# Kernel optimization log

Measured on AMD Instinct MI355X. Metric: run time of the kernel, lower is better.

## Reference

```python
import jax, jax.numpy as jnp
import numpy as np

N, K = 200000, 16
C_IN = 4           # in_channels (head stage)
H1, H2 = 16, 32    # nbr_hidden_channels//2, nbr_hidden_channels
C_OUT = 64         # channel_list[0]
HEAD = 256         # head_channels
EPS = 1e-5


def _bn(x, g, b):
    # train-mode BatchNorm1d over the row (point/neighbor) axis
    m = jnp.mean(x, axis=0)
    v = jnp.var(x, axis=0)
    return (x - m) * jax.lax.rsqrt(v + EPS) * g + b


def setup_inputs() -> dict:
    key = jax.random.key(0)
    ks = jax.random.split(key, 8)

    def lin(k, fan_in, fan_out):
        bound = 1.0 / np.sqrt(fan_in)  # torch Linear default init
        return jax.random.uniform(k, (fan_in, fan_out), minval=-bound, maxval=bound, dtype=jnp.float32)

    return {
        "p": jax.random.normal(ks[0], (N, 3), dtype=jnp.float32),
        "f": jax.random.normal(ks[1], (N, C_IN), dtype=jnp.float32),
        "group_idx": jax.random.randint(ks[2], (N, K), 0, N),
        "w1": lin(ks[3], 3 + C_IN, H1),
        "g1": jnp.ones((H1,), jnp.float32),
        "b1": jnp.zeros((H1,), jnp.float32),
        "w2": lin(ks[4], H1, H2),
        "g2": jnp.ones((H2,), jnp.float32),
        "b2": jnp.zeros((H2,), jnp.float32),
        "w3": lin(ks[5], H2, C_OUT),
        "g_nbr": 0.8 * jnp.ones((C_OUT,), jnp.float32),  # nn.init.constant_(nbr_bn.weight, 0.8)
        "b_nbr": jnp.zeros((C_OUT,), jnp.float32),
        "g_post": jnp.ones((C_OUT,), jnp.float32),       # (channel_list[0]/out_channels)**0.5 == 1.0
        "b_post": jnp.zeros((C_OUT,), jnp.float32),
        "w_post": lin(ks[6], C_OUT, HEAD),
    }


def reference(p, f, group_idx, w1, g1, b1, w2, g2, b2, w3, g_nbr, b_nbr, g_post, b_post, w_post):
    # neighbor gather: relative coords and features  -> (N, K, 3), (N, K, C_IN)
    p_nbr = p[group_idx] - p[:, None, :]
    f_nbr = f[group_idx]
    x = jnp.concatenate([p_nbr, f_nbr], axis=-1).reshape(N * K, 3 + C_IN)
    # nbr_embed: Linear-BN-GELU x2 + Linear (all no-bias linears)
    x = jax.nn.gelu(_bn(x @ w1, g1, b1), approximate=False)
    x = jax.nn.gelu(_bn(x @ w2, g2, b2), approximate=False)
    x = (x @ w3).reshape(N, K, C_OUT).max(axis=1)  # max-pool over K neighbors
    # nbr_proj is Identity for the head stage; nbr_bn then f = f_nbr
    x = _bn(x, g_nbr, b_nbr)
    # post_proj: BN + Linear(C_OUT -> HEAD, no bias)
    out = _bn(x, g_post, b_post) @ w_post
    return out
```

## Files before the change

kernel.cpp:

```cpp
#include <hip/hip_runtime.h>
#include <cmath>

#define NPTS  200000
#define KNBR  16
#define MROWS 3200000
#define EPSB  1e-5f
#define H2LD  260

__device__ __forceinline__ float gelu_f(float x) {
    return 0.5f * x * (1.0f + erff(x * 0.70710678118654752f));
}

__global__ __launch_bounds__(256) void k_pack(
    const float* __restrict__ p, const float4* __restrict__ f,
    float4* __restrict__ pk)
{
    int n = blockIdx.x * 256 + threadIdx.x;
    if (n < NPTS) {
        float4 a;
        a.x = p[n * 3 + 0]; a.y = p[n * 3 + 1]; a.z = p[n * 3 + 2]; a.w = 0.f;
        pk[2 * n]     = a;
        pk[2 * n + 1] = f[n];
    }
}

__global__ __launch_bounds__(256) void k_gy1(
    const float4* __restrict__ pk, const int* __restrict__ gidx,
    const float* __restrict__ w1, float* __restrict__ stats,
    float* __restrict__ y1d)
{
    __shared__ __align__(16) float w1s[112];
    __shared__ float red[4 * 32];
    for (int i = threadIdx.x; i < 112; i += 256) w1s[i] = w1[i];
    __syncthreads();
    const float4* w1v = (const float4*)w1s;

    float acc[32];
#pragma unroll
    for (int c = 0; c < 32; c++) acc[c] = 0.f;

    int tid = threadIdx.x;
    int lr = tid & 63;
    int stride = gridDim.x * 256;
    for (int r = blockIdx.x * 256 + tid; r < MROWS; r += stride) {
        int n = r >> 4;
        int idx = gidx[r];
        float4 pa = pk[2 * idx];
        float4 fb = pk[2 * idx + 1];
        float4 pc = pk[2 * n];
        float x[7];
        x[0] = pa.x - pc.x; x[1] = pa.y - pc.y; x[2] = pa.z - pc.z;
        x[3] = fb.x; x[4] = fb.y; x[5] = fb.z; x[6] = fb.w;
        float* yb = y1d + (size_t)(r >> 6) * 1024 + lr;
#pragma unroll
        for (int j0 = 0; j0 < 16; j0 += 4) {
            float y0 = 0.f, y1 = 0.f, y2 = 0.f, y3 = 0.f;
#pragma unroll
            for (int i = 0; i < 7; i++) {
                float4 w = w1v[i * 4 + (j0 >> 2)];
                float xi = x[i];
                y0 = fmaf(xi, w.x, y0); y1 = fmaf(xi, w.y, y1);
                y2 = fmaf(xi, w.z, y2); y3 = fmaf(xi, w.w, y3);
            }
            yb[(j0 + 0) * 64] = y0; yb[(j0 + 1) * 64] = y1;
            yb[(j0 + 2) * 64] = y2; yb[(j0 + 3) * 64] = y3;
            acc[j0 + 0] += y0; acc[16 + j0 + 0] += y0 * y0;
            acc[j0 + 1] += y1; acc[16 + j0 + 1] += y1 * y1;
            acc[j0 + 2] += y2; acc[16 + j0 + 2] += y2 * y2;
            acc[j0 + 3] += y3; acc[16 + j0 + 3] += y3 * y3;
        }
    }
    int lane = tid & 63, wv = tid >> 6;
#pragma unroll
    for (int c = 0; c < 32; c++) {
        float v = acc[c];
        v += __shfl_down(v, 32); v += __shfl_down(v, 16); v += __shfl_down(v, 8);
        v += __shfl_down(v, 4);  v += __shfl_down(v, 2);  v += __shfl_down(v, 1);
        if (lane == 0) red[wv * 32 + c] = v;
    }
    __syncthreads();
    for (int c = tid; c < 32; c += 256)
        atomicAdd(&stats[c], red[c] + red[32 + c] + red[64 + c] + red[96 + c]);
}

__global__ void k_fin1b(const float* __restrict__ stats, const float* __restrict__ g,
                        const float* __restrict__ b, float* __restrict__ scsh)
{
    int j = threadIdx.x;
    if (j < 16) {
        const float invM = 1.0f / (float)MROWS;
        float m = stats[j] * invM;
        float v = stats[16 + j] * invM - m * m;
        float sc = g[j] * rsqrtf(v + EPSB);
        scsh[j] = sc;
        scsh[16 + j] = fmaf(-m, sc, b[j]);
    }
}

__global__ __launch_bounds__(256) void k_momA(
    const float* __restrict__ y1d, const float* __restrict__ scsh1,
    float* __restrict__ stats)
{
    __shared__ float sc1s[16], sh1s[16];
    __shared__ float red[4 * 81];
    if (threadIdx.x < 16) {
        sc1s[threadIdx.x] = scsh1[threadIdx.x];
        sh1s[threadIdx.x] = scsh1[16 + threadIdx.x];
    }
    __syncthreads();

    float acc[81];
#pragma unroll
    for (int c = 0; c < 81; c++) acc[c] = 0.f;

    int tid = threadIdx.x;
    int lr = tid & 63;
    int stride = gridDim.x * 256;
    for (int r = blockIdx.x * 256 + tid; r < MROWS; r += stride) {
        const float* yb = y1d + (size_t)(r >> 6) * 1024 + lr;
        float h1[16];
#pragma unroll
        for (int j = 0; j < 16; j++)
            h1[j] = gelu_f(fmaf(yb[j * 64], sc1s[j], sh1s[j]));
        int t = 0;
#pragma unroll
        for (int i = 0; i < 6; i++)
#pragma unroll
            for (int l = i; l < 16; l++) { acc[t] = fmaf(h1[i], h1[l], acc[t]); t++; }
    }
    int lane = tid & 63, wv = tid >> 6;
#pragma unroll
    for (int c = 0; c < 81; c++) {
        float v = acc[c];
        v += __shfl_down(v, 32); v += __shfl_down(v, 16); v += __shfl_down(v, 8);
        v += __shfl_down(v, 4);  v += __shfl_down(v, 2);  v += __shfl_down(v, 1);
        if (lane == 0) red[wv * 81 + c] = v;
    }
    __syncthreads();
    for (int c = tid; c < 81; c += 256)
        atomicAdd(&stats[c], red[c] + red[81 + c] + red[162 + c] + red[243 + c]);
}

__global__ __launch_bounds__(256) void k_momB(
    const float* __restrict__ y1d, const float* __restrict__ scsh1,
    float* __restrict__ stats)
{
    __shared__ float sc1s[16], sh1s[16];
    __shared__ float red[4 * 71];
    if (threadIdx.x < 16) {
        sc1s[threadIdx.x] = scsh1[threadIdx.x];
        sh1s[threadIdx.x] = scsh1[16 + threadIdx.x];
    }
    __syncthreads();

    float acc[71];
#pragma unroll
    for (int c = 0; c < 71; c++) acc[c] = 0.f;

    int tid = threadIdx.x;
    int lr = tid & 63;
    int stride = gridDim.x * 256;
    for (int r = blockIdx.x * 256 + tid; r < MROWS; r += stride) {
        const float* yb = y1d + (size_t)(r >> 6) * 1024 + lr;
        float h1[16];
#pragma unroll
        for (int j = 0; j < 16; j++)
            h1[j] = gelu_f(fmaf(yb[j * 64], sc1s[j], sh1s[j]));
#pragma unroll
        for (int i = 0; i < 16; i++) acc[i] += h1[i];
        int t = 16;
#pragma unroll
        for (int i = 6; i < 16; i++)
#pragma unroll
            for (int l = i; l < 16; l++) { acc[t] = fmaf(h1[i], h1[l], acc[t]); t++; }
    }
    int lane = tid & 63, wv = tid >> 6;
#pragma unroll
    for (int c = 0; c < 71; c++) {
        float v = acc[c];
        v += __shfl_down(v, 32); v += __shfl_down(v, 16); v += __shfl_down(v, 8);
        v += __shfl_down(v, 4);  v += __shfl_down(v, 2);  v += __shfl_down(v, 1);
        if (lane == 0) red[wv * 71 + c] = v;
    }
    __syncthreads();
    for (int c = tid; c < 71; c += 256)
        atomicAdd(&stats[81 + c], red[c] + red[71 + c] + red[142 + c] + red[213 + c]);
}

__global__ void k_fin2(const float* __restrict__ stats, const float* __restrict__ w2,
                       const float* __restrict__ g, const float* __restrict__ b,
                       float* __restrict__ scsh)
{
    int j = threadIdx.x;
    if (j < 32) {
        const float invM = 1.0f / (float)MROWS;
        float w[16];
#pragma unroll
        for (int i = 0; i < 16; i++) w[i] = w2[i * 32 + j];
        float m = 0.f;
#pragma unroll
        for (int i = 0; i < 16; i++) m = fmaf(w[i], stats[81 + i], m);
        m *= invM;
        float e2 = 0.f;
        int t = 0;
#pragma unroll
        for (int i = 0; i < 6; i++)
#pragma unroll
            for (int l = i; l < 16; l++) {
                float coeff = (i == l) ? 1.0f : 2.0f;
                e2 = fmaf(coeff * w[i] * w[l], stats[t], e2);
                t++;
            }
        t = 97;
#pragma unroll
        for (int i = 6; i < 16; i++)
#pragma unroll
            for (int l = i; l < 16; l++) {
                float coeff = (i == l) ? 1.0f : 2.0f;
                e2 = fmaf(coeff * w[i] * w[l], stats[t], e2);
                t++;
            }
        e2 *= invM;
        float v = e2 - m * m;
        float sc = g[j] * rsqrtf(v + EPSB);
        scsh[j] = sc;
        scsh[32 + j] = fmaf(-m, sc, b[j]);
    }
}

__global__ __launch_bounds__(256) void k_pool2y(
    const float* __restrict__ y1d,
    const float* __restrict__ w2, const float* __restrict__ w3,
    const float* __restrict__ scsh1, const float* __restrict__ scsh2,
    float* __restrict__ stats, float* __restrict__ pooled)
{
    __shared__ __align__(16) float w2s[512];
    __shared__ __align__(16) float w3s[2048];
    __shared__ __align__(16) float h2t[32 * H2LD];
    __shared__ float sc1s[16], sh1s[16], sc2s[32], sh2s[32];
    __shared__ float reds[256];
    __shared__ float redq[256];
    int tid = threadIdx.x;
    for (int i = tid; i < 512; i += 256) w2s[i] = w2[i];
    for (int i = tid; i < 2048; i += 256) w3s[i] = w3[i];
    if (tid < 16) { sc1s[tid] = scsh1[tid]; sh1s[tid] = scsh1[16 + tid]; }
    if (tid < 32) { sc2s[tid] = scsh2[tid]; sh2s[tid] = scsh2[32 + tid]; }
    __syncthreads();

    const float4* w2v = (const float4*)w2s;
    const float4* w3v = (const float4*)w3s;

    int lane = tid & 63;
    int pt = tid >> 4;
    int cc = tid & 15;

    float s0 = 0.f, s1 = 0.f, s2 = 0.f, s3 = 0.f;
    float q0 = 0.f, q1 = 0.f, q2 = 0.f, q3 = 0.f;

#pragma unroll 1
    for (int it = 0; it < 4; it++) {
        int r = it * 800000 + blockIdx.x * 256 + tid;
        const float* yb = y1d + (size_t)(r >> 6) * 1024 + lane;
        float h1[16];
#pragma unroll
        for (int j = 0; j < 16; j++)
            h1[j] = gelu_f(fmaf(yb[j * 64], sc1s[j], sh1s[j]));
#pragma unroll
        for (int j0 = 0; j0 < 32; j0 += 4) {
            float y0 = 0.f, y1 = 0.f, y2 = 0.f, y3 = 0.f;
#pragma unroll
            for (int i = 0; i < 16; i++) {
                float4 w = w2v[i * 8 + (j0 >> 2)];
                float hi = h1[i];
                y0 = fmaf(hi, w.x, y0); y1 = fmaf(hi, w.y, y1);
                y2 = fmaf(hi, w.z, y2); y3 = fmaf(hi, w.w, y3);
            }
            h2t[(j0 + 0) * H2LD + tid] = gelu_f(fmaf(y0, sc2s[j0 + 0], sh2s[j0 + 0]));
            h2t[(j0 + 1) * H2LD + tid] = gelu_f(fmaf(y1, sc2s[j0 + 1], sh2s[j0 + 1]));
            h2t[(j0 + 2) * H2LD + tid] = gelu_f(fmaf(y2, sc2s[j0 + 2], sh2s[j0 + 2]));
            h2t[(j0 + 3) * H2LD + tid] = gelu_f(fmaf(y3, sc2s[j0 + 3], sh2s[j0 + 3]));
        }
        __syncthreads();

        float a[16][4];
#pragma unroll
        for (int t = 0; t < 16; t++) {
            a[t][0] = 0.f; a[t][1] = 0.f; a[t][2] = 0.f; a[t][3] = 0.f;
        }
        int rb0 = pt << 4;
#pragma unroll 8
        for (int i = 0; i < 32; i++) {
            float4 wf = w3v[i * 16 + cc];
            const float* hrow = &h2t[i * H2LD + rb0];
            float4 hA = *(const float4*)&hrow[0];
            float4 hB = *(const float4*)&hrow[4];
            float4 hC = *(const float4*)&hrow[8];
            float4 hD = *(const float4*)&hrow[12];
            float hn[16] = { hA.x, hA.y, hA.z, hA.w,
                             hB.x, hB.y, hB.z, hB.w,
                             hC.x, hC.y, hC.z, hC.w,
                             hD.x, hD.y, hD.z, hD.w };
#pragma unroll
            for (int t = 0; t < 16; t++) {
                float h = hn[t];
                a[t][0] = fmaf(h, wf.x, a[t][0]);
                a[t][1] = fmaf(h, wf.y, a[t][1]);
                a[t][2] = fmaf(h, wf.z, a[t][2]);
                a[t][3] = fmaf(h, wf.w, a[t][3]);
            }
        }
        float m0 = -3.0e38f, m1 = -3.0e38f, m2 = -3.0e38f, m3 = -3.0e38f;
#pragma unroll
        for (int t = 0; t < 16; t++) {
            m0 = fmaxf(m0, a[t][0]);
            m1 = fmaxf(m1, a[t][1]);
            m2 = fmaxf(m2, a[t][2]);
            m3 = fmaxf(m3, a[t][3]);
        }
        int np = it * 50000 + blockIdx.x * 16 + pt;
        *(float4*)&pooled[(size_t)np * 64 + cc * 4] = make_float4(m0, m1, m2, m3);
        s0 += m0; q0 = fmaf(m0, m0, q0);
        s1 += m1; q1 = fmaf(m1, m1, q1);
        s2 += m2; q2 = fmaf(m2, m2, q2);
        s3 += m3; q3 = fmaf(m3, m3, q3);
        __syncthreads();
    }

    s0 += __shfl_down(s0, 32); s0 += __shfl_down(s0, 16);
    s1 += __shfl_down(s1, 32); s1 += __shfl_down(s1, 16);
    s2 += __shfl_down(s2, 32); s2 += __shfl_down(s2, 16);
    s3 += __shfl_down(s3, 32); s3 += __shfl_down(s3, 16);
    q0 += __shfl_down(q0, 32); q0 += __shfl_down(q0, 16);
    q1 += __shfl_down(q1, 32); q1 += __shfl_down(q1, 16);
    q2 += __shfl_down(q2, 32); q2 += __shfl_down(q2, 16);
    q3 += __shfl_down(q3, 32); q3 += __shfl_down(q3, 16);
    int wv = tid >> 6;
    if (lane < 16) {
        reds[wv * 64 + lane * 4 + 0] = s0;
        reds[wv * 64 + lane * 4 + 1] = s1;
        reds[wv * 64 + lane * 4 + 2] = s2;
        reds[wv * 64 + lane * 4 + 3] = s3;
        redq[wv * 64 + lane * 4 + 0] = q0;
        redq[wv * 64 + lane * 4 + 1] = q1;
        redq[wv * 64 + lane * 4 + 2] = q2;
        redq[wv * 64 + lane * 4 + 3] = q3;
    }
    __syncthreads();
    if (tid < 64) {
        atomicAdd(&stats[tid],
                  reds[tid] + reds[64 + tid] + reds[128 + tid] + reds[192 + tid]);
        atomicAdd(&stats[64 + tid],
                  redq[tid] + redq[64 + tid] + redq[128 + tid] + redq[192 + tid]);
    }
}

__global__ __launch_bounds__(256) void k_s1g(
    const float4* __restrict__ pk, const int* __restrict__ gidx,
    float* __restrict__ stats)
{
    __shared__ float red[4 * 35];
    float acc[35];
#pragma unroll
    for (int c = 0; c < 35; c++) acc[c] = 0.f;
    int stride = gridDim.x * 256;
    for (int r = blockIdx.x * 256 + threadIdx.x; r < MROWS; r += stride) {
        int n = r >> 4;
        int idx = gidx[r];
        float4 pa = pk[2 * idx];
        float4 fb = pk[2 * idx + 1];
        float4 pc = pk[2 * n];
        float x[7];
        x[0] = pa.x - pc.x; x[1] = pa.y - pc.y; x[2] = pa.z - pc.z;
        x[3] = fb.x; x[4] = fb.y; x[5] = fb.z; x[6] = fb.w;
#pragma unroll
        for (int i = 0; i < 7; i++) acc[i] += x[i];
        int t = 7;
#pragma unroll
        for (int i = 0; i < 7; i++)
#pragma unroll
            for (int l = i; l < 7; l++) { acc[t] = fmaf(x[i], x[l], acc[t]); t++; }
    }
    int lane = threadIdx.x & 63, wv = threadIdx.x >> 6;
#pragma unroll
    for (int c = 0; c < 35; c++) {
        float v = acc[c];
        v += __shfl_down(v, 32); v += __shfl_down(v, 16); v += __shfl_down(v, 8);
        v += __shfl_down(v, 4);  v += __shfl_down(v, 2);  v += __shfl_down(v, 1);
        if (lane == 0) red[wv * 35 + c] = v;
    }
    __syncthreads();
    for (int c = threadIdx.x; c < 35; c += 256)
        atomicAdd(&stats[c], red[c] + red[35 + c] + red[70 + c] + red[105 + c]);
}

__global__ void k_f1g(const float* __restrict__ stats, const float* __restrict__ w1,
                      const float* __restrict__ g, const float* __restrict__ b,
                      float* __restrict__ scsh)
{
    int j = threadIdx.x;
    if (j < 16) {
        const float invM = 1.0f / (float)MROWS;
        float w[7];
#pragma unroll
        for (int i = 0; i < 7; i++) w[i] = w1[i * 16 + j];
        float m = 0.f;
#pragma unroll
        for (int i = 0; i < 7; i++) m = fmaf(w[i], stats[i], m);
        m *= invM;
        float e2 = 0.f;
        int t = 7;
#pragma unroll
        for (int i = 0; i < 7; i++)
#pragma unroll
            for (int l = i; l < 7; l++) {
                float coeff = (i == l) ? 1.0f : 2.0f;
                e2 = fmaf(coeff * w[i] * w[l], stats[t], e2);
                t++;
            }
        e2 *= invM;
        float v = e2 - m * m;
        float sc = g[j] * rsqrtf(v + EPSB);
        scsh[j] = sc;
        scsh[16 + j] = fmaf(-m, sc, b[j]);
    }
}

template <int PASS>
__global__ __launch_bounds__(256) void k_s2g(
    const float4* __restrict__ pk, const int* __restrict__ gidx,
    const float* __restrict__ w1, const float* __restrict__ scsh1,
    float* __restrict__ stats)
{
    constexpr int NA = (PASS == 0) ? 81 : 71;
    __shared__ __align__(16) float w1s[112];
    __shared__ float sc1s[16], sh1s[16];
    __shared__ float red[4 * NA];
    for (int i = threadIdx.x; i < 112; i += 256) w1s[i] = w1[i];
    if (threadIdx.x < 16) {
        sc1s[threadIdx.x] = scsh1[threadIdx.x];
        sh1s[threadIdx.x] = scsh1[16 + threadIdx.x];
    }
    __syncthreads();
    const float4* w1v = (const float4*)w1s;

    float acc[NA];
#pragma unroll
    for (int c = 0; c < NA; c++) acc[c] = 0.f;

    int stride = gridDim.x * 256;
    for (int r = blockIdx.x * 256 + threadIdx.x; r < MROWS; r += stride) {
        int n = r >> 4;
        int idx = gidx[r];
        float4 pa = pk[2 * idx];
        float4 fb = pk[2 * idx + 1];
        float4 pc = pk[2 * n];
        float x[7];
        x[0] = pa.x - pc.x; x[1] = pa.y - pc.y; x[2] = pa.z - pc.z;
        x[3] = fb.x; x[4] = fb.y; x[5] = fb.z; x[6] = fb.w;
        float h1[16];
#pragma unroll
        for (int j0 = 0; j0 < 16; j0 += 4) {
            float y0 = 0.f, y1 = 0.f, y2 = 0.f, y3 = 0.f;
#pragma unroll
            for (int i = 0; i < 7; i++) {
                float4 w = w1v[i * 4 + (j0 >> 2)];
                float xi = x[i];
                y0 = fmaf(xi, w.x, y0); y1 = fmaf(xi, w.y, y1);
                y2 = fmaf(xi, w.z, y2); y3 = fmaf(xi, w.w, y3);
            }
            h1[j0 + 0] = gelu_f(fmaf(y0, sc1s[j0 + 0], sh1s[j0 + 0]));
            h1[j0 + 1] = gelu_f(fmaf(y1, sc1s[j0 + 1], sh1s[j0 + 1]));
            h1[j0 + 2] = gelu_f(fmaf(y2, sc1s[j0 + 2], sh1s[j0 + 2]));
            h1[j0 + 3] = gelu_f(fmaf(y3, sc1s[j0 + 3], sh1s[j0 + 3]));
        }
        if (PASS == 0) {
            int t = 0;
#pragma unroll
            for (int i = 0; i < 6; i++)
#pragma unroll
                for (int l = i; l < 16; l++) { acc[t] = fmaf(h1[i], h1[l], acc[t]); t++; }
        } else {
#pragma unroll
            for (int i = 0; i < 16; i++) acc[i] += h1[i];
            int t = 16;
#pragma unroll
            for (int i = 6; i < 16; i++)
#pragma unroll
                for (int l = i; l < 16; l++) { acc[t] = fmaf(h1[i], h1[l], acc[t]); t++; }
        }
    }
    int lane = threadIdx.x & 63, wv = threadIdx.x >> 6;
#pragma unroll
    for (int c = 0; c < NA; c++) {
        float v = acc[c];
        v += __shfl_down(v, 32); v += __shfl_down(v, 16); v += __shfl_down(v, 8);
        v += __shfl_down(v, 4);  v += __shfl_down(v, 2);  v += __shfl_down(v, 1);
        if (lane == 0) red[wv * NA + c] = v;
    }
    __syncthreads();
    int base = (PASS == 0) ? 0 : 81;
    for (int c = threadIdx.x; c < NA; c += 256)
        atomicAdd(&stats[base + c], red[c] + red[NA + c] + red[2 * NA + c] + red[3 * NA + c]);
}

__global__ __launch_bounds__(256) void k_pool2g(
    const float* __restrict__ p, const float4* __restrict__ f,
    const int* __restrict__ gidx,
    const float* __restrict__ w1, const float* __restrict__ w2,
    const float* __restrict__ w3,
    const float* __restrict__ scsh1, const float* __restrict__ scsh2,
    float* __restrict__ stats, float* __restrict__ pooled)
{
    __shared__ __align__(16) float w1s[112];
    __shared__ __align__(16) float w2s[512];
    __shared__ __align__(16) float w3s[2048];
    __shared__ __align__(16) float h2t[32 * H2LD];
    __shared__ float sc1s[16], sh1s[16], sc2s[32], sh2s[32];
    __shared__ float reds[256];
    __shared__ float redq[256];
    int tid = threadIdx.x;
    for (int i = tid; i < 112; i += 256) w1s[i] = w1[i];
    for (int i = tid; i < 512; i += 256) w2s[i] = w2[i];
    for (int i = tid; i < 2048; i += 256) w3s[i] = w3[i];
    if (tid < 16) { sc1s[tid] = scsh1[tid]; sh1s[tid] = scsh1[16 + tid]; }
    if (tid < 32) { sc2s[tid] = scsh2[tid]; sh2s[tid] = scsh2[32 + tid]; }
    __syncthreads();

    const float4* w1v = (const float4*)w1s;
    const float4* w2v = (const float4*)w2s;
    const float4* w3v = (const float4*)w3s;

    int lane = tid & 63;
    int pt = tid >> 4;
    int cc = tid & 15;

    float s0 = 0.f, s1 = 0.f, s2 = 0.f, s3 = 0.f;
    float q0 = 0.f, q1 = 0.f, q2 = 0.f, q3 = 0.f;

#pragma unroll 1
    for (int it = 0; it < 4; it++) {
        int r = it * 800000 + blockIdx.x * 256 + tid;
        int n = r >> 4;
        int idx = gidx[r];
        float4 fv = f[idx];
        float x[7];
        x[0] = p[idx * 3 + 0] - p[n * 3 + 0];
        x[1] = p[idx * 3 + 1] - p[n * 3 + 1];
        x[2] = p[idx * 3 + 2] - p[n * 3 + 2];
        x[3] = fv.x; x[4] = fv.y; x[5] = fv.z; x[6] = fv.w;

        float h1[16];
#pragma unroll
        for (int j0 = 0; j0 < 16; j0 += 4) {
            float y0 = 0.f, y1 = 0.f, y2 = 0.f, y3 = 0.f;
#pragma unroll
            for (int i = 0; i < 7; i++) {
                float4 w = w1v[i * 4 + (j0 >> 2)];
                float xi = x[i];
                y0 = fmaf(xi, w.x, y0); y1 = fmaf(xi, w.y, y1);
                y2 = fmaf(xi, w.z, y2); y3 = fmaf(xi, w.w, y3);
            }
            h1[j0 + 0] = gelu_f(fmaf(y0, sc1s[j0 + 0], sh1s[j0 + 0]));
            h1[j0 + 1] = gelu_f(fmaf(y1, sc1s[j0 + 1], sh1s[j0 + 1]));
            h1[j0 + 2] = gelu_f(fmaf(y2, sc1s[j0 + 2], sh1s[j0 + 2]));
            h1[j0 + 3] = gelu_f(fmaf(y3, sc1s[j0 + 3], sh1s[j0 + 3]));
        }
#pragma unroll
        for (int j0 = 0; j0 < 32; j0 += 4) {
            float y0 = 0.f, y1 = 0.f, y2 = 0.f, y3 = 0.f;
#pragma unroll
            for (int i = 0; i < 16; i++) {
                float4 w = w2v[i * 8 + (j0 >> 2)];
                float hi = h1[i];
                y0 = fmaf(hi, w.x, y0); y1 = fmaf(hi, w.y, y1);
                y2 = fmaf(hi, w.z, y2); y3 = fmaf(hi, w.w, y3);
            }
            h2t[(j0 + 0) * H2LD + tid] = gelu_f(fmaf(y0, sc2s[j0 + 0], sh2s[j0 + 0]));
            h2t[(j0 + 1) * H2LD + tid] = gelu_f(fmaf(y1, sc2s[j0 + 1], sh2s[j0 + 1]));
            h2t[(j0 + 2) * H2LD + tid] = gelu_f(fmaf(y2, sc2s[j0 + 2], sh2s[j0 + 2]));
            h2t[(j0 + 3) * H2LD + tid] = gelu_f(fmaf(y3, sc2s[j0 + 3], sh2s[j0 + 3]));
        }
        __syncthreads();

        float a[16][4];
#pragma unroll
        for (int t = 0; t < 16; t++) {
            a[t][0] = 0.f; a[t][1] = 0.f; a[t][2] = 0.f; a[t][3] = 0.f;
        }
        int rb0 = pt << 4;
#pragma unroll 8
        for (int i = 0; i < 32; i++) {
            float4 wf = w3v[i * 16 + cc];
            const float* hrow = &h2t[i * H2LD + rb0];
            float4 hA = *(const float4*)&hrow[0];
            float4 hB = *(const float4*)&hrow[4];
            float4 hC = *(const float4*)&hrow[8];
            float4 hD = *(const float4*)&hrow[12];
            float hn[16] = { hA.x, hA.y, hA.z, hA.w,
                             hB.x, hB.y, hB.z, hB.w,
                             hC.x, hC.y, hC.z, hC.w,
                             hD.x, hD.y, hD.z, hD.w };
#pragma unroll
            for (int t = 0; t < 16; t++) {
                float h = hn[t];
                a[t][0] = fmaf(h, wf.x, a[t][0]);
                a[t][1] = fmaf(h, wf.y, a[t][1]);
                a[t][2] = fmaf(h, wf.z, a[t][2]);
                a[t][3] = fmaf(h, wf.w, a[t][3]);
            }
        }
        float m0 = -3.0e38f, m1 = -3.0e38f, m2 = -3.0e38f, m3 = -3.0e38f;
#pragma unroll
        for (int t = 0; t < 16; t++) {
            m0 = fmaxf(m0, a[t][0]);
            m1 = fmaxf(m1, a[t][1]);
            m2 = fmaxf(m2, a[t][2]);
            m3 = fmaxf(m3, a[t][3]);
        }
        int np = it * 50000 + blockIdx.x * 16 + pt;
        *(float4*)&pooled[(size_t)np * 64 + cc * 4] = make_float4(m0, m1, m2, m3);
        s0 += m0; q0 = fmaf(m0, m0, q0);
        s1 += m1; q1 = fmaf(m1, m1, q1);
        s2 += m2; q2 = fmaf(m2, m2, q2);
        s3 += m3; q3 = fmaf(m3, m3, q3);
        __syncthreads();
    }

    s0 += __shfl_down(s0, 32); s0 += __shfl_down(s0, 16);
    s1 += __shfl_down(s1, 32); s1 += __shfl_down(s1, 16);
    s2 += __shfl_down(s2, 32); s2 += __shfl_down(s2, 16);
    s3 += __shfl_down(s3, 32); s3 += __shfl_down(s3, 16);
    q0 += __shfl_down(q0, 32); q0 += __shfl_down(q0, 16);
    q1 += __shfl_down(q1, 32); q1 += __shfl_down(q1, 16);
    q2 += __shfl_down(q2, 32); q2 += __shfl_down(q2, 16);
    q3 += __shfl_down(q3, 32); q3 += __shfl_down(q3, 16);
    int wv = tid >> 6;
    if (lane < 16) {
        reds[wv * 64 + lane * 4 + 0] = s0;
        reds[wv * 64 + lane * 4 + 1] = s1;
        reds[wv * 64 + lane * 4 + 2] = s2;
        reds[wv * 64 + lane * 4 + 3] = s3;
        redq[wv * 64 + lane * 4 + 0] = q0;
        redq[wv * 64 + lane * 4 + 1] = q1;
        redq[wv * 64 + lane * 4 + 2] = q2;
        redq[wv * 64 + lane * 4 + 3] = q3;
    }
    __syncthreads();
    if (tid < 64) {
        atomicAdd(&stats[tid],
                  reds[tid] + reds[64 + tid] + reds[128 + tid] + reds[192 + tid]);
        atomicAdd(&stats[64 + tid],
                  redq[tid] + redq[64 + tid] + redq[128 + tid] + redq[192 + tid]);
    }
}

__global__ void k_fin3(const float* __restrict__ stats,
                       const float* __restrict__ g_nbr, const float* __restrict__ g_post,
                       const float* __restrict__ b_post, float* __restrict__ scsh)
{
    int j = threadIdx.x;
    if (j < 64) {
        float m = stats[j] * (1.0f / NPTS);
        float v = stats[64 + j] * (1.0f / NPTS) - m * m;
        float a1 = g_nbr[j] * rsqrtf(v + EPSB);
        float s3 = g_post[j] * a1 * rsqrtf(fmaf(a1 * a1, v, EPSB));
        scsh[j] = s3;
        scsh[64 + j] = fmaf(-m, s3, b_post[j]);
    }
}

__global__ __launch_bounds__(256) void k_head(
    const float* __restrict__ pooled, const float* __restrict__ scsh3,
    const float* __restrict__ wpost, float* __restrict__ out)
{
    __shared__ float rowbuf[512];
    __shared__ float s3s[64], c3s[64];
    int tid = threadIdx.x;
    if (tid < 64) { s3s[tid] = scsh3[tid]; c3s[tid] = scsh3[64 + tid]; }
    float wcol[64];
#pragma unroll
    for (int j = 0; j < 64; j++) wcol[j] = wpost[j * 256 + tid];
    __syncthreads();

    const int nchunks = NPTS / 8;
    for (int c = blockIdx.x; c < nchunks; c += gridDim.x) {
        int n0 = c * 8;
#pragma unroll
        for (int t = tid; t < 512; t += 256) {
            int rr = t >> 6, j = t & 63;
            rowbuf[t] = fmaf(pooled[(size_t)(n0 + rr) * 64 + j], s3s[j], c3s[j]);
        }
        __syncthreads();
#pragma unroll
        for (int rr = 0; rr < 8; rr++) {
            float acc = 0.f;
#pragma unroll
            for (int j = 0; j < 64; j++) acc = fmaf(rowbuf[rr * 64 + j], wcol[j], acc);
            out[(size_t)(n0 + rr) * 256 + tid] = acc;
        }
        __syncthreads();
    }
}

extern "C" void kernel_launch(void* const* d_in, const int* in_sizes, int n_in,
                              void* d_out, int out_size, void* d_ws, size_t ws_size,
                              hipStream_t stream)
{
    const float*  p    = (const float*)d_in[0];
    const float4* f    = (const float4*)d_in[1];
    const int*    gidx = (const int*)d_in[2];
    const float*  w1   = (const float*)d_in[3];
    const float*  g1   = (const float*)d_in[4];
    const float*  b1   = (const float*)d_in[5];
    const float*  w2   = (const float*)d_in[6];
    const float*  g2   = (const float*)d_in[7];
    const float*  b2   = (const float*)d_in[8];
    const float*  w3   = (const float*)d_in[9];
    const float*  gn   = (const float*)d_in[10];
    const float*  gp   = (const float*)d_in[12];
    const float*  bp   = (const float*)d_in[13];
    const float*  wp   = (const float*)d_in[14];
    float* out = (float*)d_out;
    float* ws  = (float*)d_ws;

    float* stats1 = ws;
    float* scsh1  = ws + 40;
    float* stats2 = ws + 80;
    float* scsh2  = ws + 240;
    float* stats3 = ws + 304;
    float* scsh3  = ws + 432;
    float* pooled = ws + 1024;
    float4* pk    = (float4*)(ws + 1024);
    float* y1d    = ws + 1024 + 12800000;

    const size_t need = ((size_t)1024 + 12800000 + 51200000) * 4;

    hipMemsetAsync(d_ws, 0, 2048, stream);
    k_pack<<<(NPTS + 255) / 256, 256, 0, stream>>>(p, f, pk);

    if (ws_size >= need) {
        k_gy1<<<2048, 256, 0, stream>>>(pk, gidx, w1, stats1, y1d);
        k_fin1b<<<1, 64, 0, stream>>>(stats1, g1, b1, scsh1);
        k_momA<<<2048, 256, 0, stream>>>(y1d, scsh1, stats2);
        k_momB<<<2048, 256, 0, stream>>>(y1d, scsh1, stats2);
        k_fin2<<<1, 64, 0, stream>>>(stats2, w2, g2, b2, scsh2);
        k_pool2y<<<3125, 256, 0, stream>>>(y1d, w2, w3, scsh1, scsh2, stats3, pooled);
    } else {
        k_s1g<<<2048, 256, 0, stream>>>(pk, gidx, stats1);
        k_f1g<<<1, 64, 0, stream>>>(stats1, w1, g1, b1, scsh1);
        k_s2g<0><<<2048, 256, 0, stream>>>(pk, gidx, w1, scsh1, stats2);
        k_s2g<1><<<2048, 256, 0, stream>>>(pk, gidx, w1, scsh1, stats2);
        k_fin2<<<1, 64, 0, stream>>>(stats2, w2, g2, b2, scsh2);
        k_pool2g<<<3125, 256, 0, stream>>>(p, f, gidx, w1, w2, w3, scsh1, scsh2, stats3, pooled);
    }
    k_fin3<<<1, 64, 0, stream>>>(stats3, gn, gp, bp, scsh3);
    k_head<<<1024, 256, 0, stream>>>(pooled, scsh3, wp, out);
}
```

Baseline: 1.261 ms.

## Compute BN2 stats directly from y2 in a single moment pass

Replaces the two second-moment kernels, which accumulated 152 pairwise products of h1 and were later combined with w2, with one kernel that computes y2 = h1·w2 per row and accumulates sum and sum of squares for all 32 channels. This halves the passes over the large y1 buffer and the GELU recomputation, at the cost of 512 FMAs per row instead of about 152. The finalize step becomes a generic mean/variance kernel. The pool kernels' inner FMA loop is also rewritten with a macro that reads float4s directly instead of building a temporary array.

Result: slower. 1.607 ms (+27.5%).

```diff
diff --git a/kernel.cpp b/kernel.cpp
--- a/kernel.cpp
+++ b/kernel.cpp
@@ -97,21 +97,24 @@
     }
 }
 
-__global__ __launch_bounds__(256) void k_momA(
-    const float* __restrict__ y1d, const float* __restrict__ scsh1,
-    float* __restrict__ stats)
-{
+__global__ __launch_bounds__(256) void k_momZ(
+    const float* __restrict__ y1d, const float* __restrict__ w2,
+    const float* __restrict__ scsh1, float* __restrict__ stats)
+{
+    __shared__ __align__(16) float w2s[512];
     __shared__ float sc1s[16], sh1s[16];
-    __shared__ float red[4 * 81];
+    __shared__ float red[4 * 64];
+    for (int i = threadIdx.x; i < 512; i += 256) w2s[i] = w2[i];
     if (threadIdx.x < 16) {
         sc1s[threadIdx.x] = scsh1[threadIdx.x];
         sh1s[threadIdx.x] = scsh1[16 + threadIdx.x];
     }
     __syncthreads();
-
-    float acc[81];
-#pragma unroll
-    for (int c = 0; c < 81; c++) acc[c] = 0.f;
+    const float4* w2v = (const float4*)w2s;
+
+    float acc[64];
+#pragma unroll
+    for (int c = 0; c < 64; c++) acc[c] = 0.f;
 
     int tid = threadIdx.x;
     int lr = tid & 63;
@@ -122,109 +125,46 @@
 #pragma unroll
         for (int j = 0; j < 16; j++)
             h1[j] = gelu_f(fmaf(yb[j * 64], sc1s[j], sh1s[j]));
-        int t = 0;
-#pragma unroll
-        for (int i = 0; i < 6; i++)
-#pragma unroll
-            for (int l = i; l < 16; l++) { acc[t] = fmaf(h1[i], h1[l], acc[t]); t++; }
+#pragma unroll
+        for (int j0 = 0; j0 < 32; j0 += 4) {
+            float y0 = 0.f, y1 = 0.f, y2 = 0.f, y3 = 0.f;
+#pragma unroll
+            for (int i = 0; i < 16; i++) {
+                float4 w = w2v[i * 8 + (j0 >> 2)];
+                float hi = h1[i];
+                y0 = fmaf(hi, w.x, y0); y1 = fmaf(hi, w.y, y1);
+                y2 = fmaf(hi, w.z, y2); y3 = fmaf(hi, w.w, y3);
+            }
+            acc[j0 + 0] += y0; acc[32 + j0 + 0] += y0 * y0;
+            acc[j0 + 1] += y1; acc[32 + j0 + 1] += y1 * y1;
+            acc[j0 + 2] += y2; acc[32 + j0 + 2] += y2 * y2;
+            acc[j0 + 3] += y3; acc[32 + j0 + 3] += y3 * y3;
+        }
     }
     int lane = tid & 63, wv = tid >> 6;
 #pragma unroll
-    for (int c = 0; c < 81; c++) {
+    for (int c = 0; c < 64; c++) {
         float v = acc[c];
         v += __shfl_down(v, 32); v += __shfl_down(v, 16); v += __shfl_down(v, 8);
         v += __shfl_down(v, 4);  v += __shfl_down(v, 2);  v += __shfl_down(v, 1);
-        if (lane == 0) red[wv * 81 + c] = v;
-    }
-    __syncthreads();
-    for (int c = tid; c < 81; c += 256)
-        atomicAdd(&stats[c], red[c] + red[81 + c] + red[162 + c] + red[243 + c]);
-}
-
-__global__ __launch_bounds__(256) void k_momB(
-    const float* __restrict__ y1d, const float* __restrict__ scsh1,
-    float* __restrict__ stats)
-{
-    __shared__ float sc1s[16], sh1s[16];
-    __shared__ float red[4 * 71];
-    if (threadIdx.x < 16) {
-        sc1s[threadIdx.x] = scsh1[threadIdx.x];
-        sh1s[threadIdx.x] = scsh1[16 + threadIdx.x];
-    }
-    __syncthreads();
-
-    float acc[71];
-#pragma unroll
-    for (int c = 0; c < 71; c++) acc[c] = 0.f;
-
-    int tid = threadIdx.x;
-    int lr = tid & 63;
-    int stride = gridDim.x * 256;
-    for (int r = blockIdx.x * 256 + tid; r < MROWS; r += stride) {
-        const float* yb = y1d + (size_t)(r >> 6) * 1024 + lr;
-        float h1[16];
-#pragma unroll
-        for (int j = 0; j < 16; j++)
-            h1[j] = gelu_f(fmaf(yb[j * 64], sc1s[j], sh1s[j]));
-#pragma unroll
-        for (int i = 0; i < 16; i++) acc[i] += h1[i];
-        int t = 16;
-#pragma unroll
-        for (int i = 6; i < 16; i++)
-#pragma unroll
-            for (int l = i; l < 16; l++) { acc[t] = fmaf(h1[i], h1[l], acc[t]); t++; }
-    }
-    int lane = tid & 63, wv = tid >> 6;
-#pragma unroll
-    for (int c = 0; c < 71; c++) {
-        float v = acc[c];
-        v += __shfl_down(v, 32); v += __shfl_down(v, 16); v += __shfl_down(v, 8);
-        v += __shfl_down(v, 4);  v += __shfl_down(v, 2);  v += __shfl_down(v, 1);
-        if (lane == 0) red[wv * 71 + c] = v;
-    }
-    __syncthreads();
-    for (int c = tid; c < 71; c += 256)
-        atomicAdd(&stats[81 + c], red[c] + red[71 + c] + red[142 + c] + red[213 + c]);
-}
-
-__global__ void k_fin2(const float* __restrict__ stats, const float* __restrict__ w2,
-                       const float* __restrict__ g, const float* __restrict__ b,
-                       float* __restrict__ scsh)
+        if (lane == 0) red[wv * 64 + c] = v;
+    }
+    __syncthreads();
+    for (int c = tid; c < 64; c += 256)
+        atomicAdd(&stats[c], red[c] + red[64 + c] + red[128 + c] + red[192 + c]);
+}
+
+__global__ void k_finalize(const float* __restrict__ stats, const float* __restrict__ g,
+                           const float* __restrict__ b, float* __restrict__ scsh,
+                           int H, float invM)
 {
     int j = threadIdx.x;
-    if (j < 32) {
-        const float invM = 1.0f / (float)MROWS;
-        float w[16];
-#pragma unroll
-        for (int i = 0; i < 16; i++) w[i] = w2[i * 32 + j];
-        float m = 0.f;
-#pragma unroll
-        for (int i = 0; i < 16; i++) m = fmaf(w[i], stats[81 + i], m);
-        m *= invM;
-        float e2 = 0.f;
-        int t = 0;
-#pragma unroll
-        for (int i = 0; i < 6; i++)
-#pragma unroll
-            for (int l = i; l < 16; l++) {
-                float coeff = (i == l) ? 1.0f : 2.0f;
-                e2 = fmaf(coeff * w[i] * w[l], stats[t], e2);
-                t++;
-            }
-        t = 97;
-#pragma unroll
-        for (int i = 6; i < 16; i++)
-#pragma unroll
-            for (int l = i; l < 16; l++) {
-                float coeff = (i == l) ? 1.0f : 2.0f;
-                e2 = fmaf(coeff * w[i] * w[l], stats[t], e2);
-                t++;
-            }
-        e2 *= invM;
-        float v = e2 - m * m;
+    if (j < H) {
+        float m = stats[j] * invM;
+        float v = stats[H + j] * invM - m * m;
         float sc = g[j] * rsqrtf(v + EPSB);
         scsh[j] = sc;
-        scsh[32 + j] = fmaf(-m, sc, b[j]);
+        scsh[H + j] = fmaf(-m, sc, b[j]);
     }
 }
 
@@ -288,27 +228,25 @@
             a[t][0] = 0.f; a[t][1] = 0.f; a[t][2] = 0.f; a[t][3] = 0.f;
         }
         int rb0 = pt << 4;
+#define ACC4(t, hv) \
+            a[t][0] = fmaf(hv, wf.x, a[t][0]); \
+            a[t][1] = fmaf(hv, wf.y, a[t][1]); \
+            a[t][2] = fmaf(hv, wf.z, a[t][2]); \
+            a[t][3] = fmaf(hv, wf.w, a[t][3]);
 #pragma unroll 8
         for (int i = 0; i < 32; i++) {
             float4 wf = w3v[i * 16 + cc];
-            const float* hrow = &h2t[i * H2LD + rb0];
-            float4 hA = *(const float4*)&hrow[0];
-            float4 hB = *(const float4*)&hrow[4];
-            float4 hC = *(const float4*)&hrow[8];
-            float4 hD = *(const float4*)&hrow[12];
-            float hn[16] = { hA.x, hA.y, hA.z, hA.w,
-                             hB.x, hB.y, hB.z, hB.w,
-                             hC.x, hC.y, hC.z, hC.w,
-                             hD.x, hD.y, hD.z, hD.w };
-#pragma unroll
-            for (int t = 0; t < 16; t++) {
-                float h = hn[t];
-                a[t][0] = fmaf(h, wf.x, a[t][0]);
-                a[t][1] = fmaf(h, wf.y, a[t][1]);
-                a[t][2] = fmaf(h, wf.z, a[t][2]);
-                a[t][3] = fmaf(h, wf.w, a[t][3]);
-            }
-        }
+            const float4* hp = (const float4*)&h2t[i * H2LD + rb0];
+            float4 hA = hp[0];
+            float4 hB = hp[1];
+            float4 hC = hp[2];
+            float4 hD = hp[3];
+            ACC4(0,  hA.x) ACC4(1,  hA.y) ACC4(2,  hA.z) ACC4(3,  hA.w)
+            ACC4(4,  hB.x) ACC4(5,  hB.y) ACC4(6,  hB.z) ACC4(7,  hB.w)
+            ACC4(8,  hC.x) ACC4(9,  hC.y) ACC4(10, hC.z) ACC4(11, hC.w)
+            ACC4(12, hD.x) ACC4(13, hD.y) ACC4(14, hD.z) ACC4(15, hD.w)
+        }
+#undef ACC4
         float m0 = -3.0e38f, m1 = -3.0e38f, m2 = -3.0e38f, m3 = -3.0e38f;
 #pragma unroll
         for (int t = 0; t < 16; t++) {
@@ -503,6 +441,47 @@
         atomicAdd(&stats[base + c], red[c] + red[NA + c] + red[2 * NA + c] + red[3 * NA + c]);
 }
 
+__global__ void k_fin2m(const float* __restrict__ stats, const float* __restrict__ w2,
+                        const float* __restrict__ g, const float* __restrict__ b,
+                        float* __restrict__ scsh)
+{
+    int j = threadIdx.x;
+    if (j < 32) {
+        const float invM = 1.0f / (float)MROWS;
+        float w[16];
+#pragma unroll
+        for (int i = 0; i < 16; i++) w[i] = w2[i * 32 + j];
+        float m = 0.f;
+#pragma unroll
+        for (int i = 0; i < 16; i++) m = fmaf(w[i], stats[81 + i], m);
+        m *= invM;
+        float e2 = 0.f;
+        int t = 0;
+#pragma unroll
+        for (int i = 0; i < 6; i++)
+#pragma unroll
+            for (int l = i; l < 16; l++) {
+                float coeff = (i == l) ? 1.0f : 2.0f;
+                e2 = fmaf(coeff * w[i] * w[l], stats[t], e2);
+                t++;
+            }
+        t = 97;
+#pragma unroll
+        for (int i = 6; i < 16; i++)
+#pragma unroll
+            for (int l = i; l < 16; l++) {
+                float coeff = (i == l) ? 1.0f : 2.0f;
+                e2 = fmaf(coeff * w[i] * w[l], stats[t], e2);
+                t++;
+            }
+        e2 *= invM;
+        float v = e2 - m * m;
+        float sc = g[j] * rsqrtf(v + EPSB);
+        scsh[j] = sc;
+        scsh[32 + j] = fmaf(-m, sc, b[j]);
+    }
+}
+
 __global__ __launch_bounds__(256) void k_pool2g(
     const float* __restrict__ p, const float4* __restrict__ f,
     const int* __restrict__ gidx,
@@ -588,27 +567,25 @@
             a[t][0] = 0.f; a[t][1] = 0.f; a[t][2] = 0.f; a[t][3] = 0.f;
         }
         int rb0 = pt << 4;
+#define ACC4(t, hv) \
+            a[t][0] = fmaf(hv, wf.x, a[t][0]); \
+            a[t][1] = fmaf(hv, wf.y, a[t][1]); \
+            a[t][2] = fmaf(hv, wf.z, a[t][2]); \
+            a[t][3] = fmaf(hv, wf.w, a[t][3]);
 #pragma unroll 8
         for (int i = 0; i < 32; i++) {
             float4 wf = w3v[i * 16 + cc];
-            const float* hrow = &h2t[i * H2LD + rb0];
-            float4 hA = *(const float4*)&hrow[0];
-            float4 hB = *(const float4*)&hrow[4];
-            float4 hC = *(const float4*)&hrow[8];
-            float4 hD = *(const float4*)&hrow[12];
-            float hn[16] = { hA.x, hA.y, hA.z, hA.w,
-                             hB.x, hB.y, hB.z, hB.w,
-                             hC.x, hC.y, hC.z, hC.w,
-                             hD.x, hD.y, hD.z, hD.w };
-#pragma unroll
-            for (int t = 0; t < 16; t++) {
-                float h = hn[t];
-                a[t][0] = fmaf(h, wf.x, a[t][0]);
-                a[t][1] = fmaf(h, wf.y, a[t][1]);
-                a[t][2] = fmaf(h, wf.z, a[t][2]);
-                a[t][3] = fmaf(h, wf.w, a[t][3]);
-            }
-        }
+            const float4* hp = (const float4*)&h2t[i * H2LD + rb0];
+            float4 hA = hp[0];
+            float4 hB = hp[1];
+            float4 hC = hp[2];
+            float4 hD = hp[3];
+            ACC4(0,  hA.x) ACC4(1,  hA.y) ACC4(2,  hA.z) ACC4(3,  hA.w)
+            ACC4(4,  hB.x) ACC4(5,  hB.y) ACC4(6,  hB.z) ACC4(7,  hB.w)
+            ACC4(8,  hC.x) ACC4(9,  hC.y) ACC4(10, hC.z) ACC4(11, hC.w)
+            ACC4(12, hD.x) ACC4(13, hD.y) ACC4(14, hD.z) ACC4(15, hD.w)
+        }
+#undef ACC4
         float m0 = -3.0e38f, m1 = -3.0e38f, m2 = -3.0e38f, m3 = -3.0e38f;
 #pragma unroll
         for (int t = 0; t < 16; t++) {
@@ -741,16 +718,15 @@
     if (ws_size >= need) {
         k_gy1<<<2048, 256, 0, stream>>>(pk, gidx, w1, stats1, y1d);
         k_fin1b<<<1, 64, 0, stream>>>(stats1, g1, b1, scsh1);
-        k_momA<<<2048, 256, 0, stream>>>(y1d, scsh1, stats2);
-        k_momB<<<2048, 256, 0, stream>>>(y1d, scsh1, stats2);
-        k_fin2<<<1, 64, 0, stream>>>(stats2, w2, g2, b2, scsh2);
+        k_momZ<<<2048, 256, 0, stream>>>(y1d, w2, scsh1, stats2);
+        k_finalize<<<1, 64, 0, stream>>>(stats2, g2, b2, scsh2, 32, 1.0f / (float)MROWS);
         k_pool2y<<<3125, 256, 0, stream>>>(y1d, w2, w3, scsh1, scsh2, stats3, pooled);
     } else {
         k_s1g<<<2048, 256, 0, stream>>>(pk, gidx, stats1);
         k_f1g<<<1, 64, 0, stream>>>(stats1, w1, g1, b1, scsh1);
         k_s2g<0><<<2048, 256, 0, stream>>>(pk, gidx, w1, scsh1, stats2);
         k_s2g<1><<<2048, 256, 0, stream>>>(pk, gidx, w1, scsh1, stats2);
-        k_fin2<<<1, 64, 0, stream>>>(stats2, w2, g2, b2, scsh2);
+        k_fin2m<<<1, 64, 0, stream>>>(stats2, w2, g2, b2, scsh2);
         k_pool2g<<<3125, 256, 0, stream>>>(p, f, gidx, w1, w2, w3, scsh1, scsh2, stats3, pooled);
     }
     k_fin3<<<1, 64, 0, stream>>>(stats3, gn, gp, bp, scsh3);
```
